# Kernel tuning notes

Hardware: AMD Instinct MI355X
Metric: run time of the kernel (lower is better)

## Reference

```python
import jax, jax.numpy as jnp
import numpy as np

B, N, H, NHEADS, N_COE, N_SCALES, THRE = 8, 1024, 128, 4, 50, 4, 5.0


def _layernorm(x, g, b, eps=1e-5):
    mu = x.mean(-1, keepdims=True)
    var = ((x - mu) ** 2).mean(-1, keepdims=True)
    return (x - mu) / jnp.sqrt(var + eps) * g + b


def setup_inputs() -> dict:
    key = jax.random.key(0)
    ks = jax.random.split(key, 12)

    def lin(k, out_d, in_d):
        lim = 1.0 / np.sqrt(in_d)
        kw, kb = jax.random.split(k)
        W = jax.random.uniform(kw, (out_d, in_d), minval=-lim, maxval=lim, dtype=jnp.float32)
        b = jax.random.uniform(kb, (out_d,), minval=-lim, maxval=lim, dtype=jnp.float32)
        return W, b

    eigw_W, eigw_b = lin(ks[0], H, H + 1)
    qkv_W, qkv_b = lin(ks[1], 3 * H, H)
    out_W, out_b = lin(ks[2], H, H)
    ffn1_W, ffn1_b = lin(ks[3], H, H)
    ffn2_W, ffn2_b = lin(ks[4], H, H)
    dsc_W, dsc_b = lin(ks[5], N_COE, H)
    dwav_W, dwav_b = lin(ks[6], N_COE, H)
    dscl_W, dscl_b = lin(ks[7], N_SCALES, H)
    # normalized-Laplacian eigenvalues live in [0, 2]
    eigenvalue = jax.random.uniform(ks[8], (B, N), minval=0.0, maxval=2.0, dtype=jnp.float32)
    eigenvector = jax.random.normal(ks[9], (B, N, N), dtype=jnp.float32) / np.sqrt(N)
    length = jnp.full((B,), N, dtype=jnp.int32)  # full graphs -> static shapes under jit
    return dict(
        eigenvalue=eigenvalue, eigenvector=eigenvector,
        eigw_W=eigw_W, eigw_b=eigw_b,
        ln1_g=jnp.ones((H,), jnp.float32), ln1_b=jnp.zeros((H,), jnp.float32),
        qkv_W=qkv_W, qkv_b=qkv_b, out_W=out_W, out_b=out_b,
        ln2_g=jnp.ones((H,), jnp.float32), ln2_b=jnp.zeros((H,), jnp.float32),
        ffn1_W=ffn1_W, ffn1_b=ffn1_b, ffn2_W=ffn2_W, ffn2_b=ffn2_b,
        dsc_W=dsc_W, dsc_b=dsc_b, dwav_W=dwav_W, dwav_b=dwav_b,
        dscl_W=dscl_W, dscl_b=dscl_b, length=length)


def _forward(eigenvalue, eigenvector, eigw_W, eigw_b, ln1_g, ln1_b, qkv_W, qkv_b,
             out_W, out_b, ln2_g, ln2_b, ffn1_W, ffn1_b, ffn2_W, ffn2_b,
             dsc_W, dsc_b, dwav_W, dwav_b, dscl_W, dscl_b, length):
    Bn, Nn = eigenvalue.shape
    mask1d = jnp.arange(Nn)[None, :] >= length[:, None]  # [B,N] True = padding

    # ---- SineEncoding ----
    ee = eigenvalue * 100.0
    div = jnp.exp(jnp.arange(0, H, 2, dtype=jnp.float32) * (-np.log(10000.0) / H))
    pe = ee[:, :, None] * div  # [B,N,H/2]
    eeig = jnp.concatenate([eigenvalue[:, :, None], jnp.sin(pe), jnp.cos(pe)], -1)  # [B,N,H+1]
    eig = eeig @ eigw_W.T + eigw_b  # [B,N,H]

    # ---- MHA block (pre-norm, residual) ----
    x = _layernorm(eig, ln1_g, ln1_b)
    qkv = x @ qkv_W.T + qkv_b
    q, k, v = jnp.split(qkv, 3, axis=-1)
    dh = H // NHEADS
    heads = lambda t: t.reshape(Bn, Nn, NHEADS, dh).transpose(0, 2, 1, 3)
    q, k, v = heads(q), heads(k), heads(v)
    scores = jnp.einsum('bhnd,bhmd->bhnm', q, k) / np.sqrt(dh)
    scores = jnp.where(mask1d[:, None, None, :], -1e9, scores)
    attn = jax.nn.softmax(scores, axis=-1)
    o = jnp.einsum('bhnm,bhmd->bhnd', attn, v).transpose(0, 2, 1, 3).reshape(Bn, Nn, H)
    eig = eig + (o @ out_W.T + out_b)

    # ---- FFN block (pre-norm, residual) ----
    y = _layernorm(eig, ln2_g, ln2_b)
    y = jax.nn.gelu(y @ ffn1_W.T + ffn1_b, approximate=False) @ ffn2_W.T + ffn2_b
    eig = eig + y

    # ---- decoders: masked mean-pool over eigenvalue axis ----
    len_f = length.astype(eig.dtype)[:, None] + 1e-8

    def pooled(W, b):
        c = eig @ W.T + b
        c = jnp.where(mask1d[:, :, None], 0.0, c)
        return c.sum(1) / len_f

    coe_scaling = jax.nn.sigmoid(pooled(dsc_W, dsc_b))          # [B,n_coe]
    coe_scaling = coe_scaling / (coe_scaling.sum(-1, keepdims=True) + 1e-8)
    coe_wavelet = jax.nn.sigmoid(pooled(dwav_W, dwav_b))        # [B,n_coe]
    coe_wavelet = coe_wavelet / (coe_wavelet.sum(-1, keepdims=True) + 1e-8)
    coe_scales = jax.nn.sigmoid(pooled(dscl_W, dscl_b)) * THRE  # [B,n_scales]

    # ---- Chebyshev-like recurrence (gen_base) via scan ----
    def gen_base(yv):
        te0, to0 = jnp.ones_like(yv), yv
        def step(carry, _):
            te, to = carry
            te = 2.0 * yv * to - te
            to = 2.0 * yv * te - to
            return (te, to), (te, to)
        _, (evens, odds) = jax.lax.scan(step, (te0, to0), None, length=N_COE - 1)
        wav = jnp.concatenate([te0[None], evens], 0)   # [n_coe, ...]
        scal = jnp.concatenate([to0[None], odds], 0)
        return scal, wav

    base_scaling, _ = gen_base(eigenvalue[:, :, None] - 1.0)  # [n_coe,B,N,1]
    fsw = eigenvalue[:, :, None] * coe_scales[:, None, :]     # [B,N,S]
    fsw = jnp.where(fsw > 2.0, 0.0, fsw)
    _, base_wavelet = gen_base(fsw - 1.0)                     # [n_coe,B,N,S]
    base_scaling = 0.5 * (1.0 - base_scaling)
    base_wavelet = 0.5 * (1.0 - base_wavelet)

    curr_scaling = jnp.einsum('bc,cbns->bns', coe_scaling, base_scaling)  # [B,N,1]
    curr_wavelet = jnp.einsum('bc,cbns->bns', coe_wavelet, base_wavelet)  # [B,N,S]
    fsa = jnp.concatenate([curr_scaling, curr_wavelet], -1)               # [B,N,S+1]
    # tight-frame normalization (cfg.lam.tight_use = True)
    fsa = fsa / (jnp.linalg.norm(fsa, axis=-1, keepdims=True) + 1e-8)

    # filters_i = evc @ diag(fsa[:,:,i]) @ evc^T, all scales at once
    filters = jnp.einsum('bnk,bks,bmk->bsnm', eigenvector, fsa, eigenvector)
    # F.normalize(filters) with default dim=1 -> normalize over row axis (n here)
    norm = jnp.sqrt(jnp.sum(filters ** 2, axis=2, keepdims=True))
    filters = filters / jnp.maximum(norm, 1e-12)
    # filters[edge_idx] with full lengths == flatten over (B,N,N), per scale
    bases = filters.transpose(1, 0, 2, 3).reshape(N_SCALES + 1, -1)
    return bases


def reference(eigenvalue, eigenvector, eigw_W, eigw_b, ln1_g, ln1_b, qkv_W, qkv_b,
              out_W, out_b, ln2_g, ln2_b, ffn1_W, ffn1_b, ffn2_W, ffn2_b,
              dsc_W, dsc_b, dwav_W, dwav_b, dscl_W, dscl_b, length):
    return _forward(eigenvalue, eigenvector, eigw_W, eigw_b, ln1_g, ln1_b, qkv_W, qkv_b,
                    out_W, out_b, ln2_g, ln2_b, ffn1_W, ffn1_b, ffn2_W, ffn2_b,
                    dsc_W, dsc_b, dwav_W, dwav_b, dscl_W, dscl_b, length)
```

## Files before the change

### kernel.cpp

```cpp
#include <hip/hip_runtime.h>
#include <hip/hip_bf16.h>
#include <cstdint>

#define BB 8
#define NV 1024
#define HH 128
#define DH 32
#define NCOE 50
#define NSC 4

#define WOFF_EIG 0
#define WOFF_QKV 16384
#define WOFF_OUT 65536
#define WOFF_F1  81920
#define WOFF_F2  98304
#define WB_ELEMS 114688

typedef __attribute__((ext_vector_type(8))) short short8;
typedef __attribute__((ext_vector_type(4))) float f32x4;

__device__ __forceinline__ ushort f2bf(float f) {
    uint32_t x = __float_as_uint(f);
    uint32_t r = x + 0x7FFFu + ((x >> 16) & 1u);
    return (ushort)(r >> 16);
}

#define GLDS(gp, lp) __builtin_amdgcn_global_load_lds((const __attribute__((address_space(1))) void*)(gp), (__attribute__((address_space(3))) void*)(lp), 16, 0, 0)

__global__ void k_wcvt(const float* __restrict__ eigw_W, const float* __restrict__ qkv_W,
                       const float* __restrict__ out_W, const float* __restrict__ f1W,
                       const float* __restrict__ f2W, ushort* __restrict__ Wb) {
    int idx = blockIdx.x * 256 + threadIdx.x;
    float v; int dst;
    if (idx < 16384) {
        int r = idx >> 7, k = idx & 127;
        v = eigw_W[r * 129 + 1 + k];
        dst = WOFF_EIG + (k >> 5) * 4096 + r * 32 + (k & 31);
    } else if (idx < 65536) {
        int l = idx - 16384; int c = l >> 14, rem = l & 16383;
        int r = rem >> 7, k = rem & 127;
        v = qkv_W[(size_t)(c * 128 + r) * 128 + k];
        dst = WOFF_QKV + c * 16384 + (k >> 5) * 4096 + r * 32 + (k & 31);
    } else if (idx < 81920) {
        int l = idx - 65536; int r = l >> 7, k = l & 127;
        v = out_W[r * 128 + k];
        dst = WOFF_OUT + (k >> 5) * 4096 + r * 32 + (k & 31);
    } else if (idx < 98304) {
        int l = idx - 81920; int r = l >> 7, k = l & 127;
        v = f1W[r * 128 + k];
        dst = WOFF_F1 + (k >> 5) * 4096 + r * 32 + (k & 31);
    } else {
        int l = idx - 98304; int r = l >> 7, k = l & 127;
        v = f2W[r * 128 + k];
        dst = WOFF_F2 + (k >> 5) * 4096 + r * 32 + (k & 31);
    }
    Wb[dst] = f2bf(v);
}

__global__ __launch_bounds__(256) void k_enc_sine(const float* __restrict__ ev, const ushort* __restrict__ Wb,
                                                  const float* __restrict__ eigw_W, const float* __restrict__ eigw_b,
                                                  float* __restrict__ eig) {
    __shared__ ushort As[16384];
    __shared__ ushort Bs[16384];
    int row0 = blockIdx.x * 128;
    int t = threadIdx.x, lane = t & 63, w = t >> 6;
    int wr = w >> 1, wc = w & 1;
#pragma unroll
    for (int p = 0; p < 8; ++p) {
        int ci = w * 8 + p;
        GLDS(Wb + WOFF_EIG + ci * 512 + lane * 8, Bs + ci * 512);
    }
    {
        int r = t >> 1, half = t & 1;
        float e = ev[row0 + r] * 100.0f;
#pragma unroll
        for (int ch = 0; ch < 8; ++ch) {
            short8 u;
#pragma unroll
            for (int l = 0; l < 8; ++l) {
                int j = ch * 8 + l;
                float div = expf((float)(2 * j) * -0.07195578415606394f);
                float pe = e * div;
                u[l] = (short)f2bf(half ? cosf(pe) : sinf(pe));
            }
            int k = half * 64 + ch * 8;
            *(short8*)(As + (k >> 5) * 4096 + r * 32 + (k & 31)) = u;
        }
    }
    __syncthreads();
    int cl = lane & 15, q = lane >> 4;
    f32x4 acc[4][4] = {};
#pragma unroll
    for (int kt = 0; kt < 4; ++kt) {
        const ushort* ap = As + kt * 4096 + (wr * 64 + cl) * 32 + q * 8;
        const ushort* bp = Bs + kt * 4096 + (wc * 64 + cl) * 32 + q * 8;
        short8 af[4], bfr[4];
#pragma unroll
        for (int i = 0; i < 4; ++i) af[i] = *(const short8*)(ap + i * 512);
#pragma unroll
        for (int j = 0; j < 4; ++j) bfr[j] = *(const short8*)(bp + j * 512);
#pragma unroll
        for (int i = 0; i < 4; ++i)
#pragma unroll
            for (int j = 0; j < 4; ++j)
                acc[i][j] = __builtin_amdgcn_mfma_f32_16x16x32_bf16(af[i], bfr[j], acc[i][j], 0, 0, 0);
    }
#pragma unroll
    for (int i = 0; i < 4; ++i) {
        int rbase = wr * 64 + i * 16 + q * 4;
        float er[4];
#pragma unroll
        for (int r = 0; r < 4; ++r) er[r] = ev[row0 + rbase + r];
#pragma unroll
        for (int j = 0; j < 4; ++j) {
            int col = wc * 64 + j * 16 + cl;
            float w0 = eigw_W[col * 129];
            float bv = eigw_b[col];
#pragma unroll
            for (int r = 0; r < 4; ++r)
                eig[(size_t)(row0 + rbase + r) * HH + col] = acc[i][j][r] + er[r] * w0 + bv;
        }
    }
}

__global__ __launch_bounds__(256) void k_enc_qkv(const float* __restrict__ eig, const float* __restrict__ g,
                                                 const float* __restrict__ be, const ushort* __restrict__ Wb,
                                                 const float* __restrict__ bias,
                                                 ushort* __restrict__ qb, ushort* __restrict__ kb, ushort* __restrict__ vb) {
    __shared__ ushort As[16384];
    __shared__ ushort Bs[16384];
    int row0 = blockIdx.x * 128;
    int t = threadIdx.x, lane = t & 63, w = t >> 6;
    int wr = w >> 1, wc = w & 1;
    {
        int r = t >> 1, half = t & 1;
        const float4* rowp = (const float4*)(eig + (size_t)(row0 + r) * HH + half * 64);
        float4 v[16];
        float s = 0.f, s2 = 0.f;
#pragma unroll
        for (int i = 0; i < 16; ++i) {
            float4 a = rowp[i]; v[i] = a;
            s += a.x + a.y + a.z + a.w;
            s2 += a.x * a.x + a.y * a.y + a.z * a.z + a.w * a.w;
        }
        s += __shfl_xor(s, 1); s2 += __shfl_xor(s2, 1);
        float mean = s * 0.0078125f;
        float var = s2 * 0.0078125f - mean * mean;
        float rstd = rsqrtf(var + 1e-5f);
        const float4* g4 = (const float4*)(g + half * 64);
        const float4* b4 = (const float4*)(be + half * 64);
#pragma unroll
        for (int ch = 0; ch < 8; ++ch) {
            float4 a = v[2 * ch], b2 = v[2 * ch + 1];
            float4 ga = g4[2 * ch], gb = g4[2 * ch + 1];
            float4 ba = b4[2 * ch], bb = b4[2 * ch + 1];
            short8 u;
            u[0] = (short)f2bf((a.x - mean) * rstd * ga.x + ba.x);
            u[1] = (short)f2bf((a.y - mean) * rstd * ga.y + ba.y);
            u[2] = (short)f2bf((a.z - mean) * rstd * ga.z + ba.z);
            u[3] = (short)f2bf((a.w - mean) * rstd * ga.w + ba.w);
            u[4] = (short)f2bf((b2.x - mean) * rstd * gb.x + bb.x);
            u[5] = (short)f2bf((b2.y - mean) * rstd * gb.y + bb.y);
            u[6] = (short)f2bf((b2.z - mean) * rstd * gb.z + bb.z);
            u[7] = (short)f2bf((b2.w - mean) * rstd * gb.w + bb.w);
            int k = half * 64 + ch * 8;
            *(short8*)(As + (k >> 5) * 4096 + r * 32 + (k & 31)) = u;
        }
    }
    int cl = lane & 15, q = lane >> 4;
    int bidx = row0 >> 10, nbase = row0 & (NV - 1);
    ushort* dsts[3] = {qb, kb, vb};
#pragma unroll 1
    for (int c = 0; c < 3; ++c) {
        __syncthreads();
#pragma unroll
        for (int p = 0; p < 8; ++p) {
            int ci = w * 8 + p;
            GLDS(Wb + WOFF_QKV + c * 16384 + ci * 512 + lane * 8, Bs + ci * 512);
        }
        __syncthreads();
        f32x4 acc[4][4] = {};
#pragma unroll
        for (int kt = 0; kt < 4; ++kt) {
            const ushort* ap = As + kt * 4096 + (wr * 64 + cl) * 32 + q * 8;
            const ushort* bp = Bs + kt * 4096 + (wc * 64 + cl) * 32 + q * 8;
            short8 af[4], bfr[4];
#pragma unroll
            for (int i = 0; i < 4; ++i) af[i] = *(const short8*)(ap + i * 512);
#pragma unroll
            for (int j = 0; j < 4; ++j) bfr[j] = *(const short8*)(bp + j * 512);
#pragma unroll
            for (int i = 0; i < 4; ++i)
#pragma unroll
                for (int j = 0; j < 4; ++j)
                    acc[i][j] = __builtin_amdgcn_mfma_f32_16x16x32_bf16(af[i], bfr[j], acc[i][j], 0, 0, 0);
        }
        ushort* dst = dsts[c];
#pragma unroll
        for (int j = 0; j < 4; ++j) {
            int col = wc * 64 + j * 16 + cl;
            float bv = bias[c * 128 + col];
            int h = col >> 5, dd = col & 31;
            ushort* hb = dst + ((size_t)(bidx * 4 + h) * NV + nbase) * DH + dd;
#pragma unroll
            for (int i = 0; i < 4; ++i) {
                int rbase = wr * 64 + i * 16 + q * 4;
#pragma unroll
                for (int r = 0; r < 4; ++r)
                    hb[(size_t)(rbase + r) * DH] = f2bf(acc[i][j][r] + bv);
            }
        }
    }
}

__global__ __launch_bounds__(256) void k_vt(const ushort* __restrict__ vb, ushort* __restrict__ vt) {
    __shared__ ushort Ld[256 * 40];
    int bh = blockIdx.y, n0 = blockIdx.x * 256;
    int t = threadIdx.x;
    const ushort* src = vb + ((size_t)bh * NV + n0) * DH;
#pragma unroll
    for (int p = 0; p < 4; ++p) {
        int idx = p * 256 + t;
        int rowi = idx >> 2, ch = idx & 3;
        short8 u = *(const short8*)(src + idx * 8);
        *(short8*)(&Ld[rowi * 40 + ch * 8]) = u;
    }
    __syncthreads();
    int d = t >> 3, nc = (t & 7) * 32;
    ushort* dst = vt + ((size_t)bh * DH + d) * NV + n0 + nc;
#pragma unroll
    for (int p = 0; p < 4; ++p) {
        short8 u;
#pragma unroll
        for (int i = 0; i < 8; ++i) u[i] = (short)Ld[(nc + p * 8 + i) * 40 + d];
        *(short8*)(dst + p * 8) = u;
    }
}

__global__ __launch_bounds__(256) void k_qk(const ushort* __restrict__ qb, const ushort* __restrict__ kb,
                                            float* __restrict__ S) {
    __shared__ ushort As[128 * 32];
    __shared__ ushort Bs[128 * 32];
    int tile = blockIdx.x;
    int bh = blockIdx.y;
    int n0 = (tile >> 3) * 128, m0 = (tile & 7) * 128;
    int tid = threadIdx.x, lane = tid & 63, w = tid >> 6;
    int wr = w >> 1, wc = w & 1;
    const ushort* qt = qb + ((size_t)bh * NV + n0) * DH;
    const ushort* ktb = kb + ((size_t)bh * NV + m0) * DH;
#pragma unroll
    for (int p = 0; p < 2; ++p) {
        int ci = w * 2 + p;
        GLDS(qt + ci * 512 + lane * 8, As + ci * 512);
        GLDS(ktb + ci * 512 + lane * 8, Bs + ci * 512);
    }
    __syncthreads();
    int cl = lane & 15, q = lane >> 4;
    const ushort* ap = As + ((wr * 64 + cl) * 32 + q * 8);
    const ushort* bp = Bs + ((wc * 64 + cl) * 32 + q * 8);
    short8 af[4], bfr[4];
#pragma unroll
    for (int i = 0; i < 4; ++i) af[i] = *(const short8*)(ap + i * 512);
#pragma unroll
    for (int j = 0; j < 4; ++j) bfr[j] = *(const short8*)(bp + j * 512);
    f32x4 acc[4][4] = {};
#pragma unroll
    for (int i = 0; i < 4; ++i)
#pragma unroll
        for (int j = 0; j < 4; ++j)
            acc[i][j] = __builtin_amdgcn_mfma_f32_16x16x32_bf16(af[i], bfr[j], acc[i][j], 0, 0, 0);
    size_t sb = (size_t)bh * NV * NV;
#pragma unroll
    for (int i = 0; i < 4; ++i) {
        int rbase = n0 + wr * 64 + i * 16 + q * 4;
#pragma unroll
        for (int j = 0; j < 4; ++j) {
            int col = m0 + wc * 64 + j * 16 + cl;
#pragma unroll
            for (int r = 0; r < 4; ++r)
                S[sb + (size_t)(rbase + r) * NV + col] = acc[i][j][r] * 0.17677669529663687f;
        }
    }
}

__global__ __launch_bounds__(256) void k_softmax(float* __restrict__ S) {
    __shared__ float red[4];
    int row = blockIdx.x, t = threadIdx.x, lane = t & 63;
    float* rp = S + (size_t)row * NV;
    float4 v = ((const float4*)rp)[t];
    float m = fmaxf(fmaxf(v.x, v.y), fmaxf(v.z, v.w));
#pragma unroll
    for (int off = 32; off; off >>= 1) m = fmaxf(m, __shfl_xor(m, off));
    if (lane == 0) red[t >> 6] = m;
    __syncthreads();
    m = fmaxf(fmaxf(red[0], red[1]), fmaxf(red[2], red[3]));
    __syncthreads();
    float e0 = __expf(v.x - m), e1 = __expf(v.y - m), e2 = __expf(v.z - m), e3 = __expf(v.w - m);
    float s4 = e0 + e1 + e2 + e3;
#pragma unroll
    for (int off = 32; off; off >>= 1) s4 += __shfl_xor(s4, off);
    if (lane == 0) red[t >> 6] = s4;
    __syncthreads();
    float inv = 1.0f / (red[0] + red[1] + red[2] + red[3]);
    ushort4 o;
    o.x = f2bf(e0 * inv); o.y = f2bf(e1 * inv); o.z = f2bf(e2 * inv); o.w = f2bf(e3 * inv);
    ((ushort4*)rp)[t] = o;
}

__global__ __launch_bounds__(256) void k_pv(const float* __restrict__ Sf, const ushort* __restrict__ vt,
                                            ushort* __restrict__ obuf) {
    __shared__ ushort As[128 * 32];
    __shared__ ushort Bs[32 * 32];
    int n0 = blockIdx.x * 128, bh = blockIdx.y;
    int b = bh >> 2, h = bh & 3;
    int tid = threadIdx.x, lane = tid & 63, w = tid >> 6;
    const char* Sb = (const char*)Sf;
    const ushort* vtb = vt + (size_t)bh * DH * NV;
    f32x4 acc[2][2] = {};
    for (int kt = 0; kt < NV / 32; ++kt) {
        int k0 = kt * 32;
        __syncthreads();
#pragma unroll
        for (int p = 0; p < 2; ++p) {
            int ci = w * 2 + p;
            int rrow = ci * 16 + (lane >> 2);
            int kch = (lane & 3) * 8;
            const ushort* gp = (const ushort*)(Sb + (size_t)(bh * NV + n0 + rrow) * 4096) + k0 + kch;
            GLDS(gp, As + ci * 512);
        }
        if (tid < 128) {
            int d = tid >> 2, ch = tid & 3;
            short8 u = *(const short8*)(vtb + (size_t)d * NV + k0 + ch * 8);
            *(short8*)(&Bs[d * 32 + ch * 8]) = u;
        }
        __syncthreads();
        int cl = lane & 15, q = lane >> 4;
        const ushort* ap = As + ((w * 32 + cl) * 32 + q * 8);
        const ushort* bp = Bs + (cl * 32 + q * 8);
        short8 af[2], bfr[2];
#pragma unroll
        for (int i = 0; i < 2; ++i) af[i] = *(const short8*)(ap + i * 512);
#pragma unroll
        for (int j = 0; j < 2; ++j) bfr[j] = *(const short8*)(bp + j * 512);
#pragma unroll
        for (int i = 0; i < 2; ++i)
#pragma unroll
            for (int j = 0; j < 2; ++j)
                acc[i][j] = __builtin_amdgcn_mfma_f32_16x16x32_bf16(af[i], bfr[j], acc[i][j], 0, 0, 0);
    }
    int cl = lane & 15, q = lane >> 4;
#pragma unroll
    for (int i = 0; i < 2; ++i) {
        int rbase = n0 + w * 32 + i * 16 + q * 4;
#pragma unroll
        for (int j = 0; j < 2; ++j) {
            int d = j * 16 + cl;
#pragma unroll
            for (int r = 0; r < 4; ++r)
                obuf[((size_t)(b * NV + rbase + r)) * HH + h * DH + d] = f2bf(acc[i][j][r]);
        }
    }
}

__global__ __launch_bounds__(256) void k_enc_proj(const ushort* __restrict__ obuf, const ushort* __restrict__ Wb,
                                                  const float* __restrict__ bias, float* __restrict__ eig) {
    __shared__ ushort As[16384];
    __shared__ ushort Bs[16384];
    int row0 = blockIdx.x * 128;
    int t = threadIdx.x, lane = t & 63, w = t >> 6;
    int wr = w >> 1, wc = w & 1;
#pragma unroll
    for (int p = 0; p < 8; ++p) {
        int ci = w * 8 + p;
        int kt = ci >> 3, rb = ci & 7;
        const ushort* gp = obuf + (size_t)(row0 + rb * 16 + (lane >> 2)) * HH + kt * 32 + (lane & 3) * 8;
        GLDS(gp, As + kt * 4096 + rb * 512);
        GLDS(Wb + WOFF_OUT + ci * 512 + lane * 8, Bs + ci * 512);
    }
    __syncthreads();
    int cl = lane & 15, q = lane >> 4;
    f32x4 acc[4][4] = {};
#pragma unroll
    for (int kt = 0; kt < 4; ++kt) {
        const ushort* ap = As + kt * 4096 + (wr * 64 + cl) * 32 + q * 8;
        const ushort* bp = Bs + kt * 4096 + (wc * 64 + cl) * 32 + q * 8;
        short8 af[4], bfr[4];
#pragma unroll
        for (int i = 0; i < 4; ++i) af[i] = *(const short8*)(ap + i * 512);
#pragma unroll
        for (int j = 0; j < 4; ++j) bfr[j] = *(const short8*)(bp + j * 512);
#pragma unroll
        for (int i = 0; i < 4; ++i)
#pragma unroll
            for (int j = 0; j < 4; ++j)
                acc[i][j] = __builtin_amdgcn_mfma_f32_16x16x32_bf16(af[i], bfr[j], acc[i][j], 0, 0, 0);
    }
#pragma unroll
    for (int j = 0; j < 4; ++j) {
        int col = wc * 64 + j * 16 + cl;
        float bv = bias[col];
#pragma unroll
        for (int i = 0; i < 4; ++i) {
            int rbase = wr * 64 + i * 16 + q * 4;
#pragma unroll
            for (int r = 0; r < 4; ++r) {
                size_t o = (size_t)(row0 + rbase + r) * HH + col;
                eig[o] += acc[i][j][r] + bv;
            }
        }
    }
}

__global__ __launch_bounds__(256) void k_enc_ffn(float* __restrict__ eig, const float* __restrict__ g,
                                                 const float* __restrict__ be, const ushort* __restrict__ Wb,
                                                 const float* __restrict__ b1, const float* __restrict__ b2) {
    __shared__ ushort As[16384];
    __shared__ ushort Bs[16384];
    int row0 = blockIdx.x * 128;
    int t = threadIdx.x, lane = t & 63, w = t >> 6;
    int wr = w >> 1, wc = w & 1;
    {
        int r = t >> 1, half = t & 1;
        const float4* rowp = (const float4*)(eig + (size_t)(row0 + r) * HH + half * 64);
        float4 v[16];
        float s = 0.f, s2 = 0.f;
#pragma unroll
        for (int i = 0; i < 16; ++i) {
            float4 a = rowp[i]; v[i] = a;
            s += a.x + a.y + a.z + a.w;
            s2 += a.x * a.x + a.y * a.y + a.z * a.z + a.w * a.w;
        }
        s += __shfl_xor(s, 1); s2 += __shfl_xor(s2, 1);
        float mean = s * 0.0078125f;
        float var = s2 * 0.0078125f - mean * mean;
        float rstd = rsqrtf(var + 1e-5f);
        const float4* g4 = (const float4*)(g + half * 64);
        const float4* b4 = (const float4*)(be + half * 64);
#pragma unroll
        for (int ch = 0; ch < 8; ++ch) {
            float4 a = v[2 * ch], bq = v[2 * ch + 1];
            float4 ga = g4[2 * ch], gb = g4[2 * ch + 1];
            float4 ba = b4[2 * ch], bb = b4[2 * ch + 1];
            short8 u;
            u[0] = (short)f2bf((a.x - mean) * rstd * ga.x + ba.x);
            u[1] = (short)f2bf((a.y - mean) * rstd * ga.y + ba.y);
            u[2] = (short)f2bf((a.z - mean) * rstd * ga.z + ba.z);
            u[3] = (short)f2bf((a.w - mean) * rstd * ga.w + ba.w);
            u[4] = (short)f2bf((bq.x - mean) * rstd * gb.x + bb.x);
            u[5] = (short)f2bf((bq.y - mean) * rstd * gb.y + bb.y);
            u[6] = (short)f2bf((bq.z - mean) * rstd * gb.z + bb.z);
            u[7] = (short)f2bf((bq.w - mean) * rstd * gb.w + bb.w);
            int k = half * 64 + ch * 8;
            *(short8*)(As + (k >> 5) * 4096 + r * 32 + (k & 31)) = u;
        }
    }
#pragma unroll
    for (int p = 0; p < 8; ++p) {
        int ci = w * 8 + p;
        GLDS(Wb + WOFF_F1 + ci * 512 + lane * 8, Bs + ci * 512);
    }
    __syncthreads();
    int cl = lane & 15, q = lane >> 4;
    f32x4 acc[4][4] = {};
#pragma unroll
    for (int kt = 0; kt < 4; ++kt) {
        const ushort* ap = As + kt * 4096 + (wr * 64 + cl) * 32 + q * 8;
        const ushort* bp = Bs + kt * 4096 + (wc * 64 + cl) * 32 + q * 8;
        short8 af[4], bfr[4];
#pragma unroll
        for (int i = 0; i < 4; ++i) af[i] = *(const short8*)(ap + i * 512);
#pragma unroll
        for (int j = 0; j < 4; ++j) bfr[j] = *(const short8*)(bp + j * 512);
#pragma unroll
        for (int i = 0; i < 4; ++i)
#pragma unroll
            for (int j = 0; j < 4; ++j)
                acc[i][j] = __builtin_amdgcn_mfma_f32_16x16x32_bf16(af[i], bfr[j], acc[i][j], 0, 0, 0);
    }
    __syncthreads();
#pragma unroll
    for (int j = 0; j < 4; ++j) {
        int col = wc * 64 + j * 16 + cl;
        float bv = b1[col];
        int koff = (col >> 5) * 4096 + (col & 31);
#pragma unroll
        for (int i = 0; i < 4; ++i) {
            int rbase = wr * 64 + i * 16 + q * 4;
#pragma unroll
            for (int r = 0; r < 4; ++r) {
                float a = acc[i][j][r] + bv;
                float ge = 0.5f * a * (1.0f + erff(a * 0.7071067811865475f));
                As[koff + (rbase + r) * 32] = f2bf(ge);
            }
        }
    }
#pragma unroll
    for (int p = 0; p < 8; ++p) {
        int ci = w * 8 + p;
        GLDS(Wb + WOFF_F2 + ci * 512 + lane * 8, Bs + ci * 512);
    }
    __syncthreads();
    f32x4 acc2[4][4] = {};
#pragma unroll
    for (int kt = 0; kt < 4; ++kt) {
        const ushort* ap = As + kt * 4096 + (wr * 64 + cl) * 32 + q * 8;
        const ushort* bp = Bs + kt * 4096 + (wc * 64 + cl) * 32 + q * 8;
        short8 af[4], bfr[4];
#pragma unroll
        for (int i = 0; i < 4; ++i) af[i] = *(const short8*)(ap + i * 512);
#pragma unroll
        for (int j = 0; j < 4; ++j) bfr[j] = *(const short8*)(bp + j * 512);
#pragma unroll
        for (int i = 0; i < 4; ++i)
#pragma unroll
            for (int j = 0; j < 4; ++j)
                acc2[i][j] = __builtin_amdgcn_mfma_f32_16x16x32_bf16(af[i], bfr[j], acc2[i][j], 0, 0, 0);
    }
#pragma unroll
    for (int j = 0; j < 4; ++j) {
        int col = wc * 64 + j * 16 + cl;
        float bv = b2[col];
#pragma unroll
        for (int i = 0; i < 4; ++i) {
            int rbase = wr * 64 + i * 16 + q * 4;
#pragma unroll
            for (int r = 0; r < 4; ++r) {
                size_t o = (size_t)(row0 + rbase + r) * HH + col;
                eig[o] += acc2[i][j][r] + bv;
            }
        }
    }
}

__global__ __launch_bounds__(1024) void k_meanpool(const float* __restrict__ eig, float* __restrict__ me) {
    __shared__ float part[8][HH];
    int b = blockIdx.x, t = threadIdx.x;
    int col = t & 127, grp = t >> 7;
    const float* p = eig + (size_t)b * NV * HH + (size_t)grp * 128 * HH + col;
    float s = 0.f;
    for (int n = 0; n < 128; ++n) s += p[(size_t)n * HH];
    part[grp][col] = s;
    __syncthreads();
    if (t < 128) {
        float a = 0.f;
#pragma unroll
        for (int g2 = 0; g2 < 8; ++g2) a += part[g2][t];
        me[b * HH + t] = a * (1.0f / NV);
    }
}

__global__ void k_decoders(const float* __restrict__ me,
                           const float* __restrict__ dscW, const float* __restrict__ dscb,
                           const float* __restrict__ dwavW, const float* __restrict__ dwavb,
                           const float* __restrict__ dsclW, const float* __restrict__ dsclb,
                           float* __restrict__ cs, float* __restrict__ cw, float* __restrict__ csc) {
    __shared__ float m[HH];
    __shared__ float s1[NCOE], s2[NCOE];
    __shared__ float sums[2];
    int b = blockIdx.x, t = threadIdx.x;
    m[t] = me[b * HH + t];
    m[t + 64] = me[b * HH + t + 64];
    __syncthreads();
    if (t < NCOE) {
        float a = dscb[t], a2 = dwavb[t];
        const float* w1 = dscW + t * HH;
        const float* w2 = dwavW + t * HH;
        for (int j = 0; j < HH; ++j) { a += m[j] * w1[j]; a2 += m[j] * w2[j]; }
        s1[t] = 1.f / (1.f + __expf(-a));
        s2[t] = 1.f / (1.f + __expf(-a2));
    }
    if (t < NSC) {
        float a = dsclb[t];
        const float* wv = dsclW + t * HH;
        for (int j = 0; j < HH; ++j) a += m[j] * wv[j];
        csc[b * NSC + t] = 5.0f / (1.f + __expf(-a));
    }
    __syncthreads();
    if (t == 0) {
        float a = 0.f, bb = 0.f;
        for (int c = 0; c < NCOE; ++c) { a += s1[c]; bb += s2[c]; }
        sums[0] = a; sums[1] = bb;
    }
    __syncthreads();
    if (t < NCOE) {
        cs[b * NCOE + t] = s1[t] / (sums[0] + 1e-8f);
        cw[b * NCOE + t] = s2[t] / (sums[1] + 1e-8f);
    }
}

__global__ void k_fsa(const float* __restrict__ ev, const float* __restrict__ cs,
                      const float* __restrict__ cw, const float* __restrict__ csc,
                      float* __restrict__ fsaT, float* __restrict__ fsqT) {
    __shared__ float lcs[NCOE], lcw[NCOE], lsc[NSC];
    int gid = blockIdx.x * 256 + threadIdx.x;
    int b = gid >> 10, n = gid & (NV - 1);
    int t = threadIdx.x;
    if (t < NCOE) { lcs[t] = cs[b * NCOE + t]; lcw[t] = cw[b * NCOE + t]; }
    if (t < NSC) lsc[t] = csc[b * NSC + t];
    __syncthreads();
    float e = ev[gid];
    float x = e - 1.0f;
    float te = 1.f, to = x;
    float a0 = lcs[0] * 0.5f * (1.f - to);
    for (int c = 1; c < NCOE; ++c) {
        te = 2.f * x * to - te;
        to = 2.f * x * te - to;
        a0 += lcs[c] * 0.5f * (1.f - to);
    }
    float aw[NSC];
#pragma unroll
    for (int s = 0; s < NSC; ++s) {
        float f = e * lsc[s];
        if (f > 2.0f) f = 0.0f;
        float y = f - 1.0f;
        float te2 = 1.f, to2 = y, a = 0.f;
        for (int c = 1; c < NCOE; ++c) {
            te2 = 2.f * y * to2 - te2;
            to2 = 2.f * y * te2 - to2;
            a += lcw[c] * 0.5f * (1.f - te2);
        }
        aw[s] = a;
    }
    float n2 = a0 * a0;
#pragma unroll
    for (int s = 0; s < NSC; ++s) n2 += aw[s] * aw[s];
    float inv = 1.f / (sqrtf(n2) + 1e-8f);
    float v0 = a0 * inv;
    fsaT[((size_t)b * 5 + 0) * NV + n] = v0;
    if (fsqT) fsqT[((size_t)b * 5 + 0) * NV + n] = sqrtf(fmaxf(v0, 0.f));
#pragma unroll
    for (int s = 0; s < NSC; ++s) {
        float vs = aw[s] * inv;
        fsaT[((size_t)b * 5 + 1 + s) * NV + n] = vs;
        if (fsqT) fsqT[((size_t)b * 5 + 1 + s) * NV + n] = sqrtf(fmaxf(vs, 0.f));
    }
}

__global__ void k_tobf16(const float* __restrict__ in, ushort* __restrict__ outp) {
    int i = blockIdx.x * 256 + threadIdx.x;
    const float4* p = (const float4*)in + (size_t)i * 2;
    float4 a = p[0], bq = p[1];
    uint4 r;
    r.x = (uint)f2bf(a.x) | ((uint)f2bf(a.y) << 16);
    r.y = (uint)f2bf(a.z) | ((uint)f2bf(a.w) << 16);
    r.z = (uint)f2bf(bq.x) | ((uint)f2bf(bq.y) << 16);
    r.w = (uint)f2bf(bq.z) | ((uint)f2bf(bq.w) << 16);
    ((uint4*)outp)[i] = r;
}

__global__ __launch_bounds__(256) void k_prescale(const float* __restrict__ evec, const float* __restrict__ fsq,
                                                  ushort* __restrict__ Asc) {
    int gid = blockIdx.x * 256 + threadIdx.x;
    int gk = gid & 127;
    int n = (gid >> 7) & (NV - 1);
    int b = gid >> 17;
    const float4* vp = (const float4*)(evec + ((size_t)b * NV + n) * NV + gk * 8);
    float4 a = vp[0], c = vp[1];
    int gsw = (gk & ~3) | ((gk ^ (n >> 2)) & 3);
    size_t dstbase = ((size_t)(b * 5) * NV + n) * NV + (size_t)gsw * 8;
#pragma unroll
    for (int s = 0; s < 5; ++s) {
        const float* fp = fsq + (size_t)(b * 5 + s) * NV + gk * 8;
        float4 f0 = *(const float4*)fp, f1 = *(const float4*)(fp + 4);
        uint4 r;
        r.x = (uint)f2bf(a.x * f0.x) | ((uint)f2bf(a.y * f0.y) << 16);
        r.y = (uint)f2bf(a.z * f0.z) | ((uint)f2bf(a.w * f0.w) << 16);
        r.z = (uint)f2bf(c.x * f1.x) | ((uint)f2bf(c.y * f1.y) << 16);
        r.w = (uint)f2bf(c.z * f1.z) | ((uint)f2bf(c.w * f1.w) << 16);
        *(uint4*)(Asc + dstbase + (size_t)s * NV * NV) = r;
    }
}

__global__ __launch_bounds__(256) void k_gemm_sym(const ushort* __restrict__ Asc,
                                                  float* __restrict__ out,
                                                  float* __restrict__ cn) {
    __shared__ ushort As[128 * 32];
    __shared__ ushort Bs[128 * 32];
    int lin = blockIdx.x;
    int wg = (lin & 7) * 180 + (lin >> 3);
    int bs = wg / 36, p = wg % 36;
    int b = bs / 5, s = bs % 5;
    int ti = 0, rem = p;
    while (rem >= 8 - ti) { rem -= 8 - ti; ++ti; }
    int tj = ti + rem;
    int n0 = ti * 128, m0 = tj * 128;
    int tid = threadIdx.x, lane = tid & 63, w = tid >> 6;
    int wr = w >> 1, wc = w & 1;
    const ushort* Abase = Asc + (size_t)(b * 5 + s) * NV * NV;
    int cl = lane & 15, q = lane >> 4;
    int qx = (q ^ (cl >> 2)) & 3;
    int fo = cl * 32 + qx * 8;
    f32x4 acc[4][4] = {};
    for (int kt = 0; kt < NV / 32; ++kt) {
        int k0 = kt * 32;
        __syncthreads();
#pragma unroll
        for (int p2 = 0; p2 < 2; ++p2) {
            int ci = w * 2 + p2;
            int rrow = ci * 16 + (lane >> 2);
            int kch = (lane & 3) * 8;
            GLDS(Abase + (size_t)(n0 + rrow) * NV + k0 + kch, As + ci * 512);
            GLDS(Abase + (size_t)(m0 + rrow) * NV + k0 + kch, Bs + ci * 512);
        }
        __syncthreads();
        short8 af[4], bfr[4];
#pragma unroll
        for (int i = 0; i < 4; ++i) af[i] = *(const short8*)(As + (wr * 4 + i) * 512 + fo);
#pragma unroll
        for (int j = 0; j < 4; ++j) bfr[j] = *(const short8*)(Bs + (wc * 4 + j) * 512 + fo);
#pragma unroll
        for (int i = 0; i < 4; ++i)
#pragma unroll
            for (int j = 0; j < 4; ++j)
                acc[i][j] = __builtin_amdgcn_mfma_f32_16x16x32_bf16(af[i], bfr[j], acc[i][j], 0, 0, 0);
    }
    size_t ob = (size_t)(s * BB + b) * NV * NV;
    float* cnb = cn + (size_t)(s * BB + b) * NV;
    float colss[4] = {0.f, 0.f, 0.f, 0.f};
    float rowss[4][4];
#pragma unroll
    for (int i = 0; i < 4; ++i)
#pragma unroll
        for (int r = 0; r < 4; ++r) rowss[i][r] = 0.f;
#pragma unroll
    for (int i = 0; i < 4; ++i) {
        int rbase = n0 + wr * 64 + i * 16 + q * 4;
#pragma unroll
        for (int j = 0; j < 4; ++j) {
            int col = m0 + wc * 64 + j * 16 + cl;
            float4 tv;
#pragma unroll
            for (int r = 0; r < 4; ++r) {
                float v = acc[i][j][r];
                out[ob + (size_t)(rbase + r) * NV + col] = v;
                colss[j] += v * v;
                rowss[i][r] += v * v;
                ((float*)&tv)[r] = v;
            }
            if (ti != tj) *(float4*)(out + ob + (size_t)col * NV + rbase) = tv;
        }
    }
#pragma unroll
    for (int j = 0; j < 4; ++j) {
        float v = colss[j];
        v += __shfl_xor(v, 16);
        v += __shfl_xor(v, 32);
        if (q == 0) atomicAdd(cnb + (m0 + wc * 64 + j * 16 + cl), v);
    }
    if (ti != tj) {
#pragma unroll
        for (int i = 0; i < 4; ++i)
#pragma unroll
            for (int r = 0; r < 4; ++r) {
                float v = rowss[i][r];
                v += __shfl_xor(v, 1); v += __shfl_xor(v, 2);
                v += __shfl_xor(v, 4); v += __shfl_xor(v, 8);
                if (cl == 0) atomicAdd(cnb + (n0 + wr * 64 + i * 16 + q * 4 + r), v);
            }
    }
}

__global__ __launch_bounds__(256) void k_gemm(const ushort* __restrict__ Vb,
                                              const float* __restrict__ fsaT,
                                              float* __restrict__ out,
                                              float* __restrict__ cn) {
    __shared__ ushort As[128 * 32];
    __shared__ ushort Bs[128 * 32];
    int tile = blockIdx.x;
    int bsid = blockIdx.y;
    int b = bsid / 5, s = bsid % 5;
    int n0 = (tile >> 3) * 128, m0 = (tile & 7) * 128;
    int tid = threadIdx.x, lane = tid & 63, w = tid >> 6;
    int wr = w >> 1, wc = w & 1;
    const ushort* Vbase = Vb + (size_t)b * NV * NV;
    const float* fs = fsaT + ((size_t)b * 5 + s) * NV;
    f32x4 acc[4][4] = {};

    for (int kt = 0; kt < NV / 32; ++kt) {
        int k0 = kt * 32;
        __syncthreads();
#pragma unroll
        for (int p = 0; p < 2; ++p) {
            int ci = w * 2 + p;
            int rrow = ci * 16 + (lane >> 2);
            int kch = (lane & 3) * 8;
            const ushort* gp = Vbase + (size_t)(m0 + rrow) * NV + k0 + kch;
            GLDS(gp, Bs + ci * 512);
        }
#pragma unroll
        for (int p = 0; p < 2; ++p) {
            int idx = p * 256 + tid;
            int rrow = idx >> 2;
            int kch = (idx & 3) * 8;
            const ushort* gp = Vbase + (size_t)(n0 + rrow) * NV + k0 + kch;
            uint4 raw = *(const uint4*)gp;
            const float4* fp = (const float4*)(fs + k0 + kch);
            float4 f0 = fp[0], f1 = fp[1];
            float v0 = __uint_as_float(raw.x << 16) * f0.x;
            float v1 = __uint_as_float(raw.x & 0xffff0000u) * f0.y;
            float v2 = __uint_as_float(raw.y << 16) * f0.z;
            float v3 = __uint_as_float(raw.y & 0xffff0000u) * f0.w;
            float v4 = __uint_as_float(raw.z << 16) * f1.x;
            float v5 = __uint_as_float(raw.z & 0xffff0000u) * f1.y;
            float v6 = __uint_as_float(raw.w << 16) * f1.z;
            float v7 = __uint_as_float(raw.w & 0xffff0000u) * f1.w;
            uint4 rr;
            rr.x = (uint)f2bf(v0) | ((uint)f2bf(v1) << 16);
            rr.y = (uint)f2bf(v2) | ((uint)f2bf(v3) << 16);
            rr.z = (uint)f2bf(v4) | ((uint)f2bf(v5) << 16);
            rr.w = (uint)f2bf(v6) | ((uint)f2bf(v7) << 16);
            *(uint4*)(As + rrow * 32 + kch) = rr;
        }
        __syncthreads();
        int cl = lane & 15, q = lane >> 4;
        const ushort* ap = As + ((wr * 64 + cl) * 32 + q * 8);
        const ushort* bp = Bs + ((wc * 64 + cl) * 32 + q * 8);
        short8 af[4], bfr[4];
#pragma unroll
        for (int i = 0; i < 4; ++i) af[i] = *(const short8*)(ap + i * 512);
#pragma unroll
        for (int j = 0; j < 4; ++j) bfr[j] = *(const short8*)(bp + j * 512);
#pragma unroll
        for (int i = 0; i < 4; ++i)
#pragma unroll
            for (int j = 0; j < 4; ++j)
                acc[i][j] = __builtin_amdgcn_mfma_f32_16x16x32_bf16(af[i], bfr[j], acc[i][j], 0, 0, 0);
    }
    int cl = lane & 15, q = lane >> 4;
    size_t ob = (size_t)(s * BB + b) * NV * NV;
    float colss[4] = {0.f, 0.f, 0.f, 0.f};
#pragma unroll
    for (int i = 0; i < 4; ++i) {
        int rbase = n0 + wr * 64 + i * 16 + q * 4;
#pragma unroll
        for (int j = 0; j < 4; ++j) {
            int col = m0 + wc * 64 + j * 16 + cl;
#pragma unroll
            for (int r = 0; r < 4; ++r) {
                float v = acc[i][j][r];
                out[ob + (size_t)(rbase + r) * NV + col] = v;
                colss[j] += v * v;
            }
        }
    }
    float* cnb = cn + (size_t)(s * BB + b) * NV;
#pragma unroll
    for (int j = 0; j < 4; ++j) {
        float v = colss[j];
        v += __shfl_xor(v, 16);
        v += __shfl_xor(v, 32);
        if (q == 0) atomicAdd(cnb + (m0 + wc * 64 + j * 16 + cl), v);
    }
}

__global__ void k_norm(float* __restrict__ out, const float* __restrict__ cn) {
    int bid = blockIdx.x;
    int bs = bid >> 10, n = bid & (NV - 1);
    int m4 = threadIdx.x * 4;
    float4 ssv = *(const float4*)(cn + (size_t)bs * NV + m4);
    float4* p = (float4*)(out + ((size_t)bs * NV + n) * NV + m4);
    float4 v = *p;
    v.x *= 1.f / fmaxf(sqrtf(ssv.x), 1e-12f);
    v.y *= 1.f / fmaxf(sqrtf(ssv.y), 1e-12f);
    v.z *= 1.f / fmaxf(sqrtf(ssv.z), 1e-12f);
    v.w *= 1.f / fmaxf(sqrtf(ssv.w), 1e-12f);
    *p = v;
}

extern "C" void kernel_launch(void* const* d_in, const int* in_sizes, int n_in,
                              void* d_out, int out_size, void* d_ws, size_t ws_size,
                              hipStream_t stream) {
    const float* eigenvalue = (const float*)d_in[0];
    const float* eigenvector = (const float*)d_in[1];
    const float* eigw_W = (const float*)d_in[2];
    const float* eigw_b = (const float*)d_in[3];
    const float* ln1_g = (const float*)d_in[4];
    const float* ln1_b = (const float*)d_in[5];
    const float* qkv_W = (const float*)d_in[6];
    const float* qkv_b = (const float*)d_in[7];
    const float* out_W = (const float*)d_in[8];
    const float* out_b = (const float*)d_in[9];
    const float* ln2_g = (const float*)d_in[10];
    const float* ln2_b = (const float*)d_in[11];
    const float* ffn1_W = (const float*)d_in[12];
    const float* ffn1_b = (const float*)d_in[13];
    const float* ffn2_W = (const float*)d_in[14];
    const float* ffn2_b = (const float*)d_in[15];
    const float* dsc_W = (const float*)d_in[16];
    const float* dsc_b = (const float*)d_in[17];
    const float* dwav_W = (const float*)d_in[18];
    const float* dwav_b = (const float*)d_in[19];
    const float* dscl_W = (const float*)d_in[20];
    const float* dscl_b = (const float*)d_in[21];

    char* w = (char*)d_ws;
    float* eig  = (float*)(w + 0);
    float* me   = (float*)(w + 4194304);
    float* cs   = (float*)(w + 4198400);
    float* cw   = (float*)(w + 4200448);
    float* csc  = (float*)(w + 4202496);
    float* fsaT = (float*)(w + 4203520);
    float* cn   = (float*)(w + 4367360);
    ushort* qb  = (ushort*)(w + 4531200);
    ushort* kb  = (ushort*)(w + 6628352);
    ushort* vb  = (ushort*)(w + 8725504);
    ushort* vt  = (ushort*)(w + 10822656);
    ushort* obuf = (ushort*)(w + 12919808);
    ushort* Wb  = (ushort*)(w + 15016960);
    ushort* Vb  = (ushort*)(w + 15246336);

    bool big = ws_size >= (size_t)117440512;
    float* fsqT = big ? (float*)(w + 32023552) : nullptr;
    ushort* Asc = (ushort*)(w + 33554432);

    float* outp = (float*)d_out;
    float* S = (float*)d_out;

    hipMemsetAsync(cn, 0, 40 * NV * sizeof(float), stream);

    k_wcvt<<<dim3(WB_ELEMS / 256), dim3(256), 0, stream>>>(eigw_W, qkv_W, out_W, ffn1_W, ffn2_W, Wb);
    k_enc_sine<<<dim3(64), dim3(256), 0, stream>>>(eigenvalue, Wb, eigw_W, eigw_b, eig);
    k_enc_qkv<<<dim3(64), dim3(256), 0, stream>>>(eig, ln1_g, ln1_b, Wb, qkv_b, qb, kb, vb);
    k_vt<<<dim3(4, 32), dim3(256), 0, stream>>>(vb, vt);
    k_qk<<<dim3(64, 32), dim3(256), 0, stream>>>(qb, kb, S);
    k_softmax<<<dim3(32 * NV), dim3(256), 0, stream>>>(S);
    k_pv<<<dim3(8, 32), dim3(256), 0, stream>>>(S, vt, obuf);
    k_enc_proj<<<dim3(64), dim3(256), 0, stream>>>(obuf, Wb, out_b, eig);
    k_enc_ffn<<<dim3(64), dim3(256), 0, stream>>>(eig, ln2_g, ln2_b, Wb, ffn1_b, ffn2_b);
    k_meanpool<<<dim3(BB), dim3(1024), 0, stream>>>(eig, me);
    k_decoders<<<dim3(BB), dim3(64), 0, stream>>>(me, dsc_W, dsc_b, dwav_W, dwav_b, dscl_W, dscl_b, cs, cw, csc);
    k_fsa<<<dim3(BB * NV / 256), dim3(256), 0, stream>>>(eigenvalue, cs, cw, csc, fsaT, fsqT);
    if (big) {
        k_prescale<<<dim3(BB * NV * 128 / 256), dim3(256), 0, stream>>>(eigenvector, fsqT, Asc);
        k_gemm_sym<<<dim3(36 * 40), dim3(256), 0, stream>>>(Asc, outp, cn);
    } else {
        k_tobf16<<<dim3(BB * NV * NV / (8 * 256)), dim3(256), 0, stream>>>(eigenvector, Vb);
        k_gemm<<<dim3(64, 40), dim3(256), 0, stream>>>(Vb, fsaT, outp, cn);
    }
    k_norm<<<dim3(40 * NV), dim3(256), 0, stream>>>(outp, cn);
}
```

Before: 525.4 us.

## Double-buffer symmetric GEMM LDS and move mirror-tile write into norm kernel

Double-buffers the LDS tiles in the symmetric filter GEMM so the next K-slice's global-to-LDS load is issued before the current slice's MFMAs, cutting one barrier per iteration. It also drops the strided transposed store of off-diagonal tiles from the GEMM epilogue. A new k_norm_sym kernel processes only the upper-triangular tiles: it normalizes each tile in place and writes the transposed, column-normalized mirror tile through a padded LDS transpose. This replaces the full read-modify-write normalization pass and the uncoalesced transposed stores with coalesced ones, at the cost of doubled LDS use per block.

```diff
diff --git a/kernel.cpp b/kernel.cpp
--- a/kernel.cpp
+++ b/kernel.cpp
@@ -674,8 +674,8 @@
 __global__ __launch_bounds__(256) void k_gemm_sym(const ushort* __restrict__ Asc,
                                                   float* __restrict__ out,
                                                   float* __restrict__ cn) {
-    __shared__ ushort As[128 * 32];
-    __shared__ ushort Bs[128 * 32];
+    __shared__ ushort As[2][4096];
+    __shared__ ushort Bs[2][4096];
     int lin = blockIdx.x;
     int wg = (lin & 7) * 180 + (lin >> 3);
     int bs = wg / 36, p = wg % 36;
@@ -687,27 +687,48 @@
     int tid = threadIdx.x, lane = tid & 63, w = tid >> 6;
     int wr = w >> 1, wc = w & 1;
     const ushort* Abase = Asc + (size_t)(b * 5 + s) * NV * NV;
+    const ushort* an = Abase + (size_t)n0 * NV;
+    const ushort* am = Abase + (size_t)m0 * NV;
+    int rrow0 = lane >> 2;
+    int kch = (lane & 3) * 8;
     int cl = lane & 15, q = lane >> 4;
     int qx = (q ^ (cl >> 2)) & 3;
     int fo = cl * 32 + qx * 8;
-    f32x4 acc[4][4] = {};
-    for (int kt = 0; kt < NV / 32; ++kt) {
-        int k0 = kt * 32;
-        __syncthreads();
+
+    auto STAGE = [&](int nb, int k0) {
 #pragma unroll
         for (int p2 = 0; p2 < 2; ++p2) {
             int ci = w * 2 + p2;
-            int rrow = ci * 16 + (lane >> 2);
-            int kch = (lane & 3) * 8;
-            GLDS(Abase + (size_t)(n0 + rrow) * NV + k0 + kch, As + ci * 512);
-            GLDS(Abase + (size_t)(m0 + rrow) * NV + k0 + kch, Bs + ci * 512);
-        }
+            int rr = ci * 16 + rrow0;
+            GLDS(an + (size_t)rr * NV + k0 + kch, &As[nb][ci * 512]);
+            GLDS(am + (size_t)rr * NV + k0 + kch, &Bs[nb][ci * 512]);
+        }
+    };
+
+    f32x4 acc[4][4] = {};
+    STAGE(0, 0);
+    __syncthreads();
+    for (int kt = 0; kt < 31; ++kt) {
+        int cur = kt & 1;
+        STAGE(cur ^ 1, (kt + 1) * 32);
+        short8 af[4], bfr[4];
+#pragma unroll
+        for (int i = 0; i < 4; ++i) af[i] = *(const short8*)(&As[cur][(wr * 4 + i) * 512 + fo]);
+#pragma unroll
+        for (int j = 0; j < 4; ++j) bfr[j] = *(const short8*)(&Bs[cur][(wc * 4 + j) * 512 + fo]);
+#pragma unroll
+        for (int i = 0; i < 4; ++i)
+#pragma unroll
+            for (int j = 0; j < 4; ++j)
+                acc[i][j] = __builtin_amdgcn_mfma_f32_16x16x32_bf16(af[i], bfr[j], acc[i][j], 0, 0, 0);
         __syncthreads();
+    }
+    {
         short8 af[4], bfr[4];
 #pragma unroll
-        for (int i = 0; i < 4; ++i) af[i] = *(const short8*)(As + (wr * 4 + i) * 512 + fo);
-#pragma unroll
-        for (int j = 0; j < 4; ++j) bfr[j] = *(const short8*)(Bs + (wc * 4 + j) * 512 + fo);
+        for (int i = 0; i < 4; ++i) af[i] = *(const short8*)(&As[1][(wr * 4 + i) * 512 + fo]);
+#pragma unroll
+        for (int j = 0; j < 4; ++j) bfr[j] = *(const short8*)(&Bs[1][(wc * 4 + j) * 512 + fo]);
 #pragma unroll
         for (int i = 0; i < 4; ++i)
 #pragma unroll
@@ -728,16 +749,13 @@
 #pragma unroll
         for (int j = 0; j < 4; ++j) {
             int col = m0 + wc * 64 + j * 16 + cl;
-            float4 tv;
 #pragma unroll
             for (int r = 0; r < 4; ++r) {
                 float v = acc[i][j][r];
                 out[ob + (size_t)(rbase + r) * NV + col] = v;
                 colss[j] += v * v;
                 rowss[i][r] += v * v;
-                ((float*)&tv)[r] = v;
             }
-            if (ti != tj) *(float4*)(out + ob + (size_t)col * NV + rbase) = tv;
         }
     }
 #pragma unroll
@@ -850,6 +868,56 @@
         v += __shfl_xor(v, 16);
         v += __shfl_xor(v, 32);
         if (q == 0) atomicAdd(cnb + (m0 + wc * 64 + j * 16 + cl), v);
+    }
+}
+
+__global__ __launch_bounds__(256) void k_norm_sym(float* __restrict__ out, const float* __restrict__ cn) {
+    __shared__ float L[128][68];
+    int ti = blockIdx.x >> 3, tj = blockIdx.x & 7;
+    if (ti > tj) return;
+    int bs = blockIdx.y;
+    int n0 = ti * 128, m0 = tj * 128;
+    size_t ob = (size_t)bs * NV * NV;
+    const float* cnb = cn + (size_t)bs * NV;
+    int t = threadIdx.x;
+#pragma unroll 1
+    for (int ch = 0; ch < 2; ++ch) {
+        if (ch) __syncthreads();
+#pragma unroll
+        for (int p = 0; p < 8; ++p) {
+            int idx = p * 256 + t;
+            int r = idx >> 5;
+            int c4 = (idx & 31) * 4;
+            size_t o = ob + (size_t)(n0 + ch * 64 + r) * NV + m0 + c4;
+            float4 v = *(float4*)(out + o);
+            float4 sm = *(const float4*)(cnb + m0 + c4);
+            float4 wv;
+            wv.x = v.x * (1.f / fmaxf(sqrtf(sm.x), 1e-12f));
+            wv.y = v.y * (1.f / fmaxf(sqrtf(sm.y), 1e-12f));
+            wv.z = v.z * (1.f / fmaxf(sqrtf(sm.z), 1e-12f));
+            wv.w = v.w * (1.f / fmaxf(sqrtf(sm.w), 1e-12f));
+            *(float4*)(out + o) = wv;
+            if (ti != tj) {
+                L[c4 + 0][r] = v.x; L[c4 + 1][r] = v.y;
+                L[c4 + 2][r] = v.z; L[c4 + 3][r] = v.w;
+            }
+        }
+        if (ti != tj) {
+            __syncthreads();
+#pragma unroll
+            for (int p = 0; p < 8; ++p) {
+                int idx = p * 256 + t;
+                int mr = idx >> 4;
+                int j4 = (idx & 15) * 4;
+                float4 sn = *(const float4*)(cnb + n0 + ch * 64 + j4);
+                float4 wv;
+                wv.x = L[mr][j4 + 0] * (1.f / fmaxf(sqrtf(sn.x), 1e-12f));
+                wv.y = L[mr][j4 + 1] * (1.f / fmaxf(sqrtf(sn.y), 1e-12f));
+                wv.z = L[mr][j4 + 2] * (1.f / fmaxf(sqrtf(sn.z), 1e-12f));
+                wv.w = L[mr][j4 + 3] * (1.f / fmaxf(sqrtf(sn.w), 1e-12f));
+                *(float4*)(out + ob + (size_t)(m0 + mr) * NV + n0 + ch * 64 + j4) = wv;
+            }
+        }
     }
 }
 
@@ -933,9 +1001,10 @@
     if (big) {
         k_prescale<<<dim3(BB * NV * 128 / 256), dim3(256), 0, stream>>>(eigenvector, fsqT, Asc);
         k_gemm_sym<<<dim3(36 * 40), dim3(256), 0, stream>>>(Asc, outp, cn);
+        k_norm_sym<<<dim3(64, 40), dim3(256), 0, stream>>>(outp, cn);
     } else {
         k_tobf16<<<dim3(BB * NV * NV / (8 * 256)), dim3(256), 0, stream>>>(eigenvector, Vb);
         k_gemm<<<dim3(64, 40), dim3(256), 0, stream>>>(Vb, fsaT, outp, cn);
-    }
-    k_norm<<<dim3(40 * NV), dim3(256), 0, stream>>>(outp, cn);
-}
+        k_norm<<<dim3(40 * NV), dim3(256), 0, stream>>>(outp, cn);
+    }
+}
```

Measured after the change: 525.9 us. About the same (+0.1%).
